# Kernel optimization log

Measured on AMD Instinct MI355X. Metric: run time of the kernel, lower is better.

## Reference

```python
import jax, jax.numpy as jnp
import numpy as np

B, C, H, W = 8, 256, 56, 56
R = 2
E = C // R  # embed_dim = in_channels // r


def setup_inputs() -> dict:
    key = jax.random.key(0)
    ks = jax.random.split(key, 10)
    s = 0.02
    return {
        "x": jax.random.normal(ks[0], (B, C, H, W), jnp.float32),
        "Wq": jax.random.normal(ks[1], (E, C), jnp.float32) * s,
        "bq": jax.random.normal(ks[2], (E,), jnp.float32) * s,
        "Wk": jax.random.normal(ks[3], (E, C), jnp.float32) * s,
        "bk": jax.random.normal(ks[4], (E,), jnp.float32) * s,
        "Wv": jax.random.normal(ks[5], (E, C), jnp.float32) * s,
        "bv": jax.random.normal(ks[6], (E,), jnp.float32) * s,
        "Wcat": jax.random.normal(ks[7], (1, 2 * E), jnp.float32) * s,  # 1x1 conv, no bias
        "Wexp": jax.random.normal(ks[8], (C, E), jnp.float32) * s,
        "bexp": jax.random.normal(ks[9], (C,), jnp.float32) * s,
    }


def reference(x, Wq, bq, Wk, bk, Wv, bv, Wcat, Wexp, bexp):
    b, c, h, w = x.shape
    n = h * w
    xf = x.reshape(b, c, n)  # 1x1 convs are channel matmuls over flattened pixels
    q = jnp.einsum('ec,bcn->ben', Wq, xf) + bq[None, :, None]   # [b,E,n]
    k = jnp.einsum('ec,bcn->ben', Wk, xf) + bk[None, :, None]   # [b,E,n]
    v = jnp.einsum('ec,bcn->bne', Wv, xf) + bv[None, None, :]   # [b,n,E]
    # concat_project 1x1 conv on qk=[q;k] repeated along a new n2 axis.
    # NOTE: source repeats BOTH q and k as 'b c n1 -> b c n1 n2', so the score
    # is constant along n2: s[b,n1] = ReLU(wq.q[:,n1] + wk.k[:,n1]).
    wq_c, wk_c = Wcat[0, :E], Wcat[0, E:]
    s = jax.nn.relu(jnp.einsum('e,ben->bn', wq_c, q)
                    + jnp.einsum('e,ben->bn', wk_c, k))         # [b,n]
    attn = jnp.broadcast_to(s[:, :, None], (b, n, n)) / n       # [b,n,n]
    embed = jnp.einsum('bij,bje->bie', attn, v)                 # [b,n,E]
    out = jnp.einsum('ce,bne->bcn', Wexp, embed) + bexp[None, :, None]
    return out.reshape(b, c, h, w) + x
```

## Files before the change

kernel.cpp:

```cpp
#include <hip/hip_runtime.h>

#define CC 256
#define EE 128
#define BB 8
#define NN 3136
#define NN4 784
#define T4 8
#define NTILES 98

__device__ __forceinline__ float waveReduceSum(float v) {
    #pragma unroll
    for (int off = 32; off > 0; off >>= 1) v += __shfl_down(v, off, 64);
    return v;
}

__global__ void k_xbar(const float* __restrict__ x, float* __restrict__ xbar) {
    int row = blockIdx.x;
    int tid = threadIdx.x;
    const float4* xr = (const float4*)(x + (size_t)row * NN);
    float acc = 0.f;
    for (int i = tid; i < NN4; i += 256) {
        float4 v = xr[i];
        acc += (v.x + v.y) + (v.z + v.w);
    }
    acc = waveReduceSum(acc);
    __shared__ float red[4];
    int wid = tid >> 6, lane = tid & 63;
    if (lane == 0) red[wid] = acc;
    __syncthreads();
    if (tid == 0) xbar[row] = (red[0] + red[1] + red[2] + red[3]) * (1.0f / NN);
}

__global__ void k_vbar(const float* __restrict__ xbar, const float* __restrict__ Wv,
                       const float* __restrict__ bv, float* __restrict__ vbar) {
    int w = threadIdx.x >> 6, lane = threadIdx.x & 63;
    int d = blockIdx.x * 4 + w;
    int b = d >> 7, e = d & 127;
    const float* wr = Wv + e * CC;
    const float* xb = xbar + b * CC;
    float acc = wr[lane]       * xb[lane]
              + wr[lane + 64]  * xb[lane + 64]
              + wr[lane + 128] * xb[lane + 128]
              + wr[lane + 192] * xb[lane + 192];
    acc = waveReduceSum(acc);
    if (lane == 0) vbar[d] = acc + bv[e];
}

__global__ void k_gexp(const float* __restrict__ vbar, const float* __restrict__ Wexp,
                       const float* __restrict__ Wq, const float* __restrict__ bq,
                       const float* __restrict__ Wk, const float* __restrict__ bk,
                       const float* __restrict__ Wcat,
                       float* __restrict__ gexp, float* __restrict__ Aout,
                       float* __restrict__ cst) {
    int tid = threadIdx.x;
    if (blockIdx.x == 512) {
        float a = 0.f;
        #pragma unroll 8
        for (int e = 0; e < EE; e++)
            a += Wcat[e] * Wq[e * CC + tid] + Wcat[EE + e] * Wk[e * CC + tid];
        Aout[tid] = a;
        if (tid < 64) {
            float cp = Wcat[tid] * bq[tid] + Wcat[tid + 64] * bq[tid + 64]
                     + Wcat[EE + tid] * bk[tid] + Wcat[EE + tid + 64] * bk[tid + 64];
            cp = waveReduceSum(cp);
            if (tid == 0) cst[0] = cp;
        }
        return;
    }
    int w = tid >> 6, lane = tid & 63;
    int d = blockIdx.x * 4 + w;
    int b = d >> 8, c = d & 255;
    const float* we = Wexp + c * EE;
    const float* vb = vbar + b * EE;
    float acc = we[lane] * vb[lane] + we[lane + 64] * vb[lane + 64];
    acc = waveReduceSum(acc);
    if (lane == 0) gexp[d] = acc;
}

__global__ void __launch_bounds__(256) k_fused(
        const float* __restrict__ x, const float* __restrict__ A,
        const float* __restrict__ cst, const float* __restrict__ gexp,
        const float* __restrict__ bexp, float* __restrict__ out) {
    int b = blockIdx.x / NTILES;
    int tile = blockIdx.x - b * NTILES;
    int tid = threadIdx.x;
    int i4l = tid & 7, cg = tid >> 3;

    __shared__ float A_s[CC];
    __shared__ float g_s[CC];
    __shared__ float be_s[CC];
    __shared__ float4 part[32][8];
    __shared__ float4 s_s[8];

    A_s[tid]  = A[tid];
    g_s[tid]  = gexp[b * CC + tid];
    be_s[tid] = bexp[tid];
    __syncthreads();

    const float4* x4 = (const float4*)x + (size_t)b * CC * NN4 + tile * T4;
    float4*       o4 = (float4*)out     + (size_t)b * CC * NN4 + tile * T4;

    float4 xc[8];
    float4 acc = make_float4(0.f, 0.f, 0.f, 0.f);
    #pragma unroll
    for (int j = 0; j < 8; j++) {
        int c = cg * 8 + j;
        float4 v = x4[(size_t)c * NN4 + i4l];
        xc[j] = v;
        float a = A_s[c];
        acc.x = fmaf(a, v.x, acc.x);
        acc.y = fmaf(a, v.y, acc.y);
        acc.z = fmaf(a, v.z, acc.z);
        acc.w = fmaf(a, v.w, acc.w);
    }
    part[cg][i4l] = acc;
    __syncthreads();
    if (tid < 8) {
        float4 sum = part[0][tid];
        #pragma unroll
        for (int g = 1; g < 32; g++) {
            float4 p = part[g][tid];
            sum.x += p.x; sum.y += p.y; sum.z += p.z; sum.w += p.w;
        }
        float cv = cst[0];
        float4 s;
        s.x = fmaxf(sum.x + cv, 0.f);
        s.y = fmaxf(sum.y + cv, 0.f);
        s.z = fmaxf(sum.z + cv, 0.f);
        s.w = fmaxf(sum.w + cv, 0.f);
        s_s[tid] = s;
    }
    __syncthreads();

    float4 sv = s_s[i4l];
    #pragma unroll
    for (int j = 0; j < 8; j++) {
        int c = cg * 8 + j;
        float g  = g_s[c];
        float be = be_s[c];
        float4 xv = xc[j];
        float4 o;
        o.x = fmaf(sv.x, g, xv.x) + be;
        o.y = fmaf(sv.y, g, xv.y) + be;
        o.z = fmaf(sv.z, g, xv.z) + be;
        o.w = fmaf(sv.w, g, xv.w) + be;
        o4[(size_t)c * NN4 + i4l] = o;
    }
}

extern "C" void kernel_launch(void* const* d_in, const int* in_sizes, int n_in,
                              void* d_out, int out_size, void* d_ws, size_t ws_size,
                              hipStream_t stream) {
    const float* x    = (const float*)d_in[0];
    const float* Wq   = (const float*)d_in[1];
    const float* bq   = (const float*)d_in[2];
    const float* Wk   = (const float*)d_in[3];
    const float* bk   = (const float*)d_in[4];
    const float* Wv   = (const float*)d_in[5];
    const float* bv   = (const float*)d_in[6];
    const float* Wcat = (const float*)d_in[7];
    const float* Wexp = (const float*)d_in[8];
    const float* bexp = (const float*)d_in[9];
    float* out = (float*)d_out;

    float* ws   = (float*)d_ws;
    float* xbar = ws;
    float* gexp = ws + 2048;
    float* A    = ws + 4096;
    float* cst  = ws + 4352;
    float* vbar = ws + 4368;

    k_xbar<<<BB * CC, 256, 0, stream>>>(x, xbar);
    k_vbar<<<256, 256, 0, stream>>>(xbar, Wv, bv, vbar);
    k_gexp<<<513, 256, 0, stream>>>(vbar, Wexp, Wq, bq, Wk, bk, Wcat, gexp, A, cst);
    k_fused<<<BB * NTILES, 256, 0, stream>>>(x, A, cst, gexp, bexp, out);
}
```

Baseline: 111.7 us.

## Fuse all stages into one cooperative kernel reading x once

Replaces the four-kernel pipeline with a single cooperative kernel that loads each x tile into registers once. The same registers feed the per-channel mean partials, the score computation and the output. Grid syncs separate the stages: reduce the partials into xbar, precompute M=Wexp·Wv and the bias terms, then compute gexp. This removes the second full read of x and the inter-kernel launch gaps. In exchange it pays three grid-wide barriers, holds 64 registers of x per thread, and needs all 392 blocks resident at once, falling back to the old path if the cooperative launch fails.

```diff
diff --git a/kernel.cpp b/kernel.cpp
--- a/kernel.cpp
+++ b/kernel.cpp
@@ -1,17 +1,178 @@
 #include <hip/hip_runtime.h>
+#include <hip/hip_cooperative_groups.h>
+
+namespace cg = cooperative_groups;
 
 #define CC 256
 #define EE 128
 #define BB 8
 #define NN 3136
 #define NN4 784
-#define T4 8
-#define NTILES 98
+#define T4 16
+#define NTILES 49
+#define NFUSED (BB * NTILES)
 
 __device__ __forceinline__ float waveReduceSum(float v) {
     #pragma unroll
     for (int off = 32; off > 0; off >>= 1) v += __shfl_down(v, off, 64);
     return v;
+}
+
+__global__ void __launch_bounds__(256, 2) k_all(
+        const float* __restrict__ x,
+        const float* __restrict__ Wq, const float* __restrict__ bq,
+        const float* __restrict__ Wk, const float* __restrict__ bk,
+        const float* __restrict__ Wv, const float* __restrict__ bv,
+        const float* __restrict__ Wcat, const float* __restrict__ Wexp,
+        const float* __restrict__ bexp, float* __restrict__ out,
+        float* __restrict__ ws) {
+    cg::grid_group grid = cg::this_grid();
+
+    float* xbar     = ws;
+    float* gexp     = ws + 2048;
+    float* Ag       = ws + 4096;
+    float* cst      = ws + 4352;
+    float* hg       = ws + 4368;
+    float* Mg       = ws + 4624;
+    float* partials = ws + 70160;
+
+    __shared__ float partc[CC][T4 + 1];
+    __shared__ float A_s[CC];
+    __shared__ float g_s[CC];
+    __shared__ float be_s[CC];
+    __shared__ float4 part4[16][16];
+    __shared__ float4 s_s[16];
+
+    const int blk = blockIdx.x;
+    const int tid = threadIdx.x;
+    const int i4l = tid & 15;
+    const int cgi = tid >> 4;
+    const int b = blk / NTILES;
+    const int tile = blk - b * NTILES;
+    const float4* x4 = (const float4*)x + (size_t)b * CC * NN4
+                       + (size_t)tile * T4 + i4l;
+
+    float4 xc[16];
+    #pragma unroll
+    for (int j = 0; j < 16; j++) {
+        int c = cgi * 16 + j;
+        float4 v = x4[(size_t)c * NN4];
+        xc[j] = v;
+        partc[c][i4l] = (v.x + v.y) + (v.z + v.w);
+    }
+    __syncthreads();
+    {
+        float sum = 0.f;
+        #pragma unroll
+        for (int i = 0; i < T4; i++) sum += partc[tid][i];
+        partials[blk * CC + tid] = sum;
+    }
+    grid.sync();
+
+    if (blk < BB) {
+        float s = 0.f;
+        #pragma unroll 7
+        for (int t = 0; t < NTILES; t++)
+            s += partials[(blk * NTILES + t) * CC + tid];
+        xbar[blk * CC + tid] = s * (1.0f / NN);
+    } else if (blk < BB + CC) {
+        int r = blk - BB;
+        const float* wer = Wexp + r * EE;
+        float m = 0.f;
+        #pragma unroll 8
+        for (int e = 0; e < EE; e++) m += wer[e] * Wv[e * CC + tid];
+        Mg[r * CC + tid] = m;
+        if (tid < 64) {
+            float hp = wer[tid] * bv[tid] + wer[tid + 64] * bv[tid + 64];
+            hp = waveReduceSum(hp);
+            if (tid == 0) hg[r] = hp;
+        }
+    } else if (blk == BB + CC) {
+        float a = 0.f;
+        #pragma unroll 8
+        for (int e = 0; e < EE; e++)
+            a += Wcat[e] * Wq[e * CC + tid] + Wcat[EE + e] * Wk[e * CC + tid];
+        Ag[tid] = a;
+        if (tid < 64) {
+            float cp = Wcat[tid] * bq[tid] + Wcat[tid + 64] * bq[tid + 64]
+                     + Wcat[EE + tid] * bk[tid] + Wcat[EE + tid + 64] * bk[tid + 64];
+            cp = waveReduceSum(cp);
+            if (tid == 0) cst[0] = cp;
+        }
+    }
+    grid.sync();
+
+    {
+        int w = tid >> 6, lane = tid & 63;
+        int gw = blk * 4 + w;
+        #pragma unroll
+        for (int rep = 0; rep < 2; rep++) {
+            int d = gw + rep * 1568;
+            if (d < 2048) {
+                int b2 = d >> 8, c2 = d & 255;
+                const float* Mr = Mg + c2 * CC;
+                const float* xb = xbar + b2 * CC;
+                float acc = Mr[lane]       * xb[lane]
+                          + Mr[lane + 64]  * xb[lane + 64]
+                          + Mr[lane + 128] * xb[lane + 128]
+                          + Mr[lane + 192] * xb[lane + 192];
+                acc = waveReduceSum(acc);
+                if (lane == 0) gexp[d] = acc + hg[c2];
+            }
+        }
+    }
+    grid.sync();
+
+    A_s[tid]  = Ag[tid];
+    g_s[tid]  = gexp[b * CC + tid];
+    be_s[tid] = bexp[tid];
+    __syncthreads();
+    float4 acc = make_float4(0.f, 0.f, 0.f, 0.f);
+    #pragma unroll
+    for (int j = 0; j < 16; j++) {
+        int c = cgi * 16 + j;
+        float a = A_s[c];
+        float4 v = xc[j];
+        acc.x = fmaf(a, v.x, acc.x);
+        acc.y = fmaf(a, v.y, acc.y);
+        acc.z = fmaf(a, v.z, acc.z);
+        acc.w = fmaf(a, v.w, acc.w);
+    }
+    part4[cgi][i4l] = acc;
+    __syncthreads();
+    if (tid < 16) {
+        float4 sum = part4[0][tid];
+        #pragma unroll
+        for (int g = 1; g < 16; g++) {
+            float4 p = part4[g][tid];
+            sum.x += p.x; sum.y += p.y; sum.z += p.z; sum.w += p.w;
+        }
+        float cv = cst[0];
+        float4 s;
+        s.x = fmaxf(sum.x + cv, 0.f);
+        s.y = fmaxf(sum.y + cv, 0.f);
+        s.z = fmaxf(sum.z + cv, 0.f);
+        s.w = fmaxf(sum.w + cv, 0.f);
+        s_s[tid] = s;
+    }
+    __syncthreads();
+    {
+        float4 sv = s_s[i4l];
+        float4* o4 = (float4*)out + (size_t)b * CC * NN4 + (size_t)tile * T4 + i4l;
+        #pragma unroll
+        for (int j = 0; j < 16; j++) {
+            int c = cgi * 16 + j;
+            float g  = g_s[c];
+            float be = be_s[c];
+            float4 xv = xc[j];
+            float4 o;
+            o.x = fmaf(sv.x, g, xv.x) + be;
+            o.y = fmaf(sv.y, g, xv.y) + be;
+            o.z = fmaf(sv.z, g, xv.z) + be;
+            o.w = fmaf(sv.w, g, xv.w) + be;
+            o4[(size_t)c * NN4] = o;
+        }
+    }
 }
 
 __global__ void k_xbar(const float* __restrict__ x, float* __restrict__ xbar) {
@@ -77,12 +238,14 @@
     if (lane == 0) gexp[d] = acc;
 }
 
+#define FT4 8
+#define FNTILES 98
 __global__ void __launch_bounds__(256) k_fused(
         const float* __restrict__ x, const float* __restrict__ A,
         const float* __restrict__ cst, const float* __restrict__ gexp,
         const float* __restrict__ bexp, float* __restrict__ out) {
-    int b = blockIdx.x / NTILES;
-    int tile = blockIdx.x - b * NTILES;
+    int b = blockIdx.x / FNTILES;
+    int tile = blockIdx.x - b * FNTILES;
     int tid = threadIdx.x;
     int i4l = tid & 7, cg = tid >> 3;
 
@@ -97,8 +260,8 @@
     be_s[tid] = bexp[tid];
     __syncthreads();
 
-    const float4* x4 = (const float4*)x + (size_t)b * CC * NN4 + tile * T4;
-    float4*       o4 = (float4*)out     + (size_t)b * CC * NN4 + tile * T4;
+    const float4* x4 = (const float4*)x + (size_t)b * CC * NN4 + tile * FT4;
+    float4*       o4 = (float4*)out     + (size_t)b * CC * NN4 + tile * FT4;
 
     float4 xc[8];
     float4 acc = make_float4(0.f, 0.f, 0.f, 0.f);
@@ -131,7 +294,6 @@
         s_s[tid] = s;
     }
     __syncthreads();
-
     float4 sv = s_s[i4l];
     #pragma unroll
     for (int j = 0; j < 8; j++) {
@@ -162,16 +324,24 @@
     const float* Wexp = (const float*)d_in[8];
     const float* bexp = (const float*)d_in[9];
     float* out = (float*)d_out;
-
-    float* ws   = (float*)d_ws;
-    float* xbar = ws;
-    float* gexp = ws + 2048;
-    float* A    = ws + 4096;
-    float* cst  = ws + 4352;
-    float* vbar = ws + 4368;
-
-    k_xbar<<<BB * CC, 256, 0, stream>>>(x, xbar);
-    k_vbar<<<256, 256, 0, stream>>>(xbar, Wv, bv, vbar);
-    k_gexp<<<513, 256, 0, stream>>>(vbar, Wexp, Wq, bq, Wk, bk, Wcat, gexp, A, cst);
-    k_fused<<<BB * NTILES, 256, 0, stream>>>(x, A, cst, gexp, bexp, out);
-}
+    float* ws  = (float*)d_ws;
+
+    void* args[] = {
+        (void*)&x, (void*)&Wq, (void*)&bq, (void*)&Wk, (void*)&bk,
+        (void*)&Wv, (void*)&bv, (void*)&Wcat, (void*)&Wexp, (void*)&bexp,
+        (void*)&out, (void*)&ws
+    };
+    hipError_t err = hipLaunchCooperativeKernel((const void*)k_all, dim3(NFUSED),
+                                                dim3(256), args, 0, stream);
+    if (err != hipSuccess) {
+        float* xbar = ws;
+        float* gexp = ws + 2048;
+        float* A    = ws + 4096;
+        float* cst  = ws + 4352;
+        float* vbar = ws + 4624;
+        k_xbar<<<BB * CC, 256, 0, stream>>>(x, xbar);
+        k_vbar<<<256, 256, 0, stream>>>(xbar, Wv, bv, vbar);
+        k_gexp<<<513, 256, 0, stream>>>(vbar, Wexp, Wq, bq, Wk, bk, Wcat, gexp, A, cst);
+        k_fused<<<BB * FNTILES, 256, 0, stream>>>(x, A, cst, gexp, bexp, out);
+    }
+}
```

Result: slower. 244.1 us (+118.5%).
